# Optimization experiments

Hardware: AMD Instinct MI355X
Metric: run time of the kernel (lower is better)

The kernel has to match this reference:

```python
import jax, jax.numpy as jnp
import numpy as np


def setup_inputs() -> dict:
    key = jax.random.key(0)
    k1, k2, k3, k4 = jax.random.split(key, 4)
    B, S, D_in, D_state, D_out = 8, 2048, 1024, 1024, 1024
    x = jax.random.normal(k1, (B, S, D_in), dtype=jnp.float32)
    # A ~ rand * 0.1 (as in torch init)
    A = jax.random.uniform(k2, (D_state,), dtype=jnp.float32) * 0.1
    # B.weight ~ U(-0.01, 0.01)
    B_w = jax.random.uniform(k3, (D_state, D_in), dtype=jnp.float32, minval=-0.01, maxval=0.01)
    # linear_out: default torch Linear init (kaiming-uniform-ish); just use small uniform
    bound = 1.0 / np.sqrt(D_state)
    kw, kb = jax.random.split(k4)
    Wo = jax.random.uniform(kw, (D_out, D_state), dtype=jnp.float32, minval=-bound, maxval=bound)
    bo = jax.random.uniform(kb, (D_out,), dtype=jnp.float32, minval=-bound, maxval=bound)
    return {"x": x, "A": A, "B_w": B_w, "Wo": Wo, "bo": bo}


def reference(x, A, B_w, Wo, bo):
    # x: (B, S, D_in)
    Bsz = x.shape[0]
    D_state = A.shape[0]
    exp_decay = jnp.exp(-jnp.minimum(A, 10.0))  # (D_state,)
    # Precompute input projection in one batched matmul: (B, S, D_state)
    Bx = jnp.einsum("bsi,ni->bsn", x, B_w)

    def step(state, bx_t):
        # state: (B, D_state); bx_t: (B, D_state)
        state = jnp.tanh(exp_decay * state + bx_t)
        return state, state

    init = jnp.zeros((Bsz, D_state), dtype=x.dtype)
    # scan over time axis: move S to leading axis
    _, h = jax.lax.scan(step, init, jnp.swapaxes(Bx, 0, 1))  # h: (S, B, D_state)
    h = jnp.swapaxes(h, 0, 1)  # (B, S, D_state)
    out = jnp.einsum("bsn,on->bso", h, Wo) + bo
    return out
```

## Files before the change

### kernel.cpp

```cpp
#include <hip/hip_runtime.h>
#include <stdint.h>


typedef __attribute__((ext_vector_type(8))) short bf16x8;
typedef __attribute__((ext_vector_type(4))) float f32x4;
typedef __attribute__((ext_vector_type(8))) unsigned short u16x8;

#define C2F 2.88539008177792681472f
#define LOG2E 1.44269504088896340736f

static __device__ __forceinline__ unsigned short f2b(float f) {
  unsigned u = __builtin_bit_cast(unsigned, f);
  unsigned r = 0x7FFFu + ((u >> 16) & 1u);
  return (unsigned short)((u + r) >> 16);
}

static __device__ __forceinline__ void gload_lds16(const void* g, void* l) {
  __builtin_amdgcn_global_load_lds(
      (const __attribute__((address_space(1))) void*)(uintptr_t)g,
      (__attribute__((address_space(3))) void*)(unsigned)(uintptr_t)l,
      16, 0, 0);
}

__global__ __launch_bounds__(256) void cvt_f32_bf16(const float* __restrict__ in,
                                                    unsigned short* __restrict__ out,
                                                    float scale, int n8) {
  int i = blockIdx.x * 256 + threadIdx.x;
  if (i >= n8) return;
  const float4* p = (const float4*)in;
  float4 v0 = p[2 * (size_t)i];
  float4 v1 = p[2 * (size_t)i + 1];
  u16x8 o;
  o[0] = f2b(v0.x * scale); o[1] = f2b(v0.y * scale);
  o[2] = f2b(v0.z * scale); o[3] = f2b(v0.w * scale);
  o[4] = f2b(v1.x * scale); o[5] = f2b(v1.y * scale);
  o[6] = f2b(v1.z * scale); o[7] = f2b(v1.w * scale);
  *(u16x8*)(out + 8 * (size_t)i) = o;
}

__global__ __launch_bounds__(256) void dkc_kernel(const float* __restrict__ Av,
                                                  float* __restrict__ dkc, int n) {
  int i = blockIdx.x * 256 + threadIdx.x;
  if (i >= n) return;
  float a = fminf(Av[i], 10.0f);
  dkc[i] = C2F * __builtin_amdgcn_exp2f(-a * LOG2E);
}

__global__ __launch_bounds__(256) void bias2_kernel(const float* __restrict__ Wo,
                                                    const float* __restrict__ bo,
                                                    float* __restrict__ bias2) {
  const int o = blockIdx.x * 4 + (threadIdx.x >> 6);
  const int lane = threadIdx.x & 63;
  const float4* row = (const float4*)(Wo + (size_t)o * 1024);
  float s = 0.0f;
#pragma unroll
  for (int k = 0; k < 4; ++k) {
    float4 v = row[lane + k * 64];
    s += v.x + v.y + v.z + v.w;
  }
#pragma unroll
  for (int off = 32; off; off >>= 1) s += __shfl_down(s, off);
  if (lane == 0) bias2[o] = s + bo[o];
}

template <int MODE>
__global__ __launch_bounds__(512, 1) void gemm256(const unsigned short* __restrict__ A,
                                                  const unsigned short* __restrict__ B,
                                                  float* __restrict__ C,
                                                  const float* __restrict__ bv,
                                                  int M, int N, int K) {
  constexpr int BK = 32;
  __shared__ char lds[4][2][16384];
  const int tid = threadIdx.x;
  const int wave = tid >> 6, lane = tid & 63;
  const int wr = wave >> 2, wc = wave & 3;

  const int nbn = N >> 8;
  const int per = gridDim.x >> 3;
  const int tilei = (blockIdx.x & 7) * per + (blockIdx.x >> 3);
  const int m0 = (tilei / nbn) << 8;
  const int n0 = (tilei % nbn) << 8;

  int soff[2];
#pragma unroll
  for (int i = 0; i < 2; ++i) {
    int o = i * 8192 + wave * 1024 + lane * 16;
    int rp = o >> 7;
    int p = ((o >> 4) & 7) ^ (rp & 7);
    int row = rp * 2 + (p >> 2);
    int chunk = p & 3;
    soff[i] = row * K + chunk * 8;
  }
  const unsigned short* Abase = A + (size_t)m0 * K;
  const unsigned short* Bbase = B + (size_t)n0 * K;

#define STAGE(T_)                                                                \
  {                                                                              \
    const int _buf = (T_) & 3;                                                   \
    const int _k0 = (T_) * BK;                                                   \
    _Pragma("unroll") for (int i = 0; i < 2; ++i) {                              \
      gload_lds16(Abase + _k0 + soff[i], &lds[_buf][0][i * 8192 + wave * 1024]); \
      gload_lds16(Bbase + _k0 + soff[i], &lds[_buf][1][i * 8192 + wave * 1024]); \
    }                                                                            \
  }

  const int l15 = lane & 15, ck = lane >> 4;
  const int ra = wr * 128 + l15;
  const int rb = wc * 64 + l15;
  const int baseA = (ra >> 1) * 128 + ((((ra & 1) << 2) + ck) ^ ((ra >> 1) & 7)) * 16;
  const int baseB = (rb >> 1) * 128 + ((((rb & 1) << 2) + ck) ^ ((rb >> 1) & 7)) * 16;

  f32x4 acc[8][4] = {};

  STAGE(0); STAGE(1); STAGE(2);

  const int T = K / BK;

#define ITER(T_, WAITN, DOSTAGE)                                                  \
  {                                                                               \
    if (DOSTAGE) STAGE((T_) + 3);                                                 \
    asm volatile("s_waitcnt vmcnt(" #WAITN ")" ::: "memory");                     \
    __builtin_amdgcn_s_barrier();                                                 \
    const char* pa = &lds[(T_) & 3][0][baseA];                                    \
    const char* pb = &lds[(T_) & 3][1][baseB];                                    \
    bf16x8 bfr[4], af[4];                                                         \
    _Pragma("unroll") for (int nf = 0; nf < 4; ++nf)                              \
        bfr[nf] = *(const bf16x8*)(pb + nf * 1024);                               \
    _Pragma("unroll") for (int mf = 0; mf < 4; ++mf)                              \
        af[mf] = *(const bf16x8*)(pa + mf * 1024);                                \
    __builtin_amdgcn_s_setprio(1);                                                \
    _Pragma("unroll") for (int mf = 0; mf < 4; ++mf)                              \
      _Pragma("unroll") for (int nf = 0; nf < 4; ++nf)                            \
        acc[mf][nf] = __builtin_amdgcn_mfma_f32_16x16x32_bf16(af[mf], bfr[nf],    \
                                                              acc[mf][nf], 0, 0, 0); \
    __builtin_amdgcn_s_setprio(0);                                                \
    _Pragma("unroll") for (int mf = 0; mf < 4; ++mf)                              \
        af[mf] = *(const bf16x8*)(pa + (mf + 4) * 1024);                          \
    __builtin_amdgcn_s_setprio(1);                                                \
    _Pragma("unroll") for (int mf = 0; mf < 4; ++mf)                              \
      _Pragma("unroll") for (int nf = 0; nf < 4; ++nf)                            \
        acc[mf + 4][nf] = __builtin_amdgcn_mfma_f32_16x16x32_bf16(                \
            af[mf], bfr[nf], acc[mf + 4][nf], 0, 0, 0);                           \
    __builtin_amdgcn_s_setprio(0);                                                \
    __builtin_amdgcn_s_barrier();                                                 \
  }

  for (int t = 0; t < T - 3; ++t) ITER(t, 12, 1);
  ITER(T - 3, 8, 0);
  ITER(T - 2, 4, 0);
  ITER(T - 1, 0, 0);
#undef ITER
#undef STAGE

  const int cr = (lane >> 4) * 4;
  const int cc = lane & 15;
#pragma unroll
  for (int nf = 0; nf < 4; ++nf) {
    const int gc = n0 + wc * 64 + nf * 16 + cc;
    const float b = bv[gc];
#pragma unroll
    for (int mf = 0; mf < 8; ++mf) {
      const size_t base = (size_t)(m0 + wr * 128 + mf * 16 + cr) * N + gc;
#pragma unroll
      for (int r = 0; r < 4; ++r) {
        float v = MODE == 0 ? fmaf(acc[mf][nf][r], C2F, b) : (acc[mf][nf][r] + b);
        C[base + (size_t)r * N] = v;
      }
    }
  }
}

__global__ __launch_bounds__(256) void scan_kernel(const float* __restrict__ Bx,
                                                   const float* __restrict__ Av,
                                                   unsigned short* __restrict__ h) {
  constexpr int S = 2048, D = 1024, CHUNK = 256, W = 384;
  const int bid = blockIdx.x;
  const int half = bid & 1;
  const int chunk = (bid >> 1) & 7;
  const int b = bid >> 4;
  const int p = half * 256 + threadIdx.x;
  const unsigned n0 = 2u * p;

  const float2 av = *(const float2*)(Av + n0);
  const float m2dk0 = -2.0f * C2F * __builtin_amdgcn_exp2f(-fminf(av.x, 10.0f) * LOG2E);
  const float m2dk1 = -2.0f * C2F * __builtin_amdgcn_exp2f(-fminf(av.y, 10.0f) * LOG2E);

  const unsigned base = (unsigned)b * (S * D) + n0;
  const int t_store0 = chunk * CHUNK;
  const int t_start = (chunk * CHUNK - W) < 0 ? 0 : (chunk * CHUNK - W);
  const int t_end = t_store0 + CHUNK;

  float2 A[8], Bf[8];
#pragma unroll
  for (int j = 0; j < 8; ++j) A[j] = *(const float2*)(Bx + base + (unsigned)(t_start + j) * D);
#pragma unroll
  for (int j = 0; j < 8; ++j) Bf[j] = *(const float2*)(Bx + base + (unsigned)(t_start + 8 + j) * D);

  float r0 = 0.5f, r1 = 0.5f;

#define STEP2(CV)                                         \
  {                                                       \
    float w0 = fmaf(m2dk0, r0, (CV).x);                   \
    float w1 = fmaf(m2dk1, r1, (CV).y);                   \
    float e0 = __builtin_amdgcn_exp2f(w0);                \
    float e1 = __builtin_amdgcn_exp2f(w1);                \
    r0 = __builtin_amdgcn_rcpf(e0 + 1.0f);                \
    r1 = __builtin_amdgcn_rcpf(e1 + 1.0f);                \
  }

#define STORE2(T_)                                                        \
  {                                                                       \
    unsigned pk;                                                          \
    asm("v_cvt_pk_bf16_f32 %0, %1, %2" : "=v"(pk) : "v"(r0), "v"(r1));    \
    *(unsigned*)(h + base + (unsigned)(T_) * D) = pk;                     \
  }

  for (int t0 = t_start; t0 < t_store0; t0 += 16) {
#pragma unroll
    for (int j = 0; j < 8; ++j) STEP2(A[j]);
#pragma unroll
    for (int j = 0; j < 8; ++j) A[j] = *(const float2*)(Bx + base + (unsigned)(t0 + 16 + j) * D);
#pragma unroll
    for (int j = 0; j < 8; ++j) STEP2(Bf[j]);
#pragma unroll
    for (int j = 0; j < 8; ++j) Bf[j] = *(const float2*)(Bx + base + (unsigned)(t0 + 24 + j) * D);
  }
  for (int t0 = t_store0; t0 < t_end; t0 += 16) {
#pragma unroll
    for (int j = 0; j < 8; ++j) { STEP2(A[j]); STORE2(t0 + j); }
    if (t0 + 16 < t_end) {
#pragma unroll
      for (int j = 0; j < 8; ++j) A[j] = *(const float2*)(Bx + base + (unsigned)(t0 + 16 + j) * D);
    }
#pragma unroll
    for (int j = 0; j < 8; ++j) { STEP2(Bf[j]); STORE2(t0 + 8 + j); }
    if (t0 + 24 < t_end) {
#pragma unroll
      for (int j = 0; j < 8; ++j) Bf[j] = *(const float2*)(Bx + base + (unsigned)(t0 + 24 + j) * D);
    }
  }
#undef STEP2
#undef STORE2
}

extern "C" void kernel_launch(void* const* d_in, const int* in_sizes, int n_in,
                              void* d_out, int out_size, void* d_ws, size_t ws_size,
                              hipStream_t stream) {
  const float* x  = (const float*)d_in[0];
  const float* Av = (const float*)d_in[1];
  const float* Bw = (const float*)d_in[2];
  const float* Wo = (const float*)d_in[3];
  const float* bo = (const float*)d_in[4];
  float* out = (float*)d_out;

  const int Bsz = 8, S = 2048, Din = 1024, Dst = 1024, Dout = 1024;
  const int M = Bsz * S;

  char* ws = (char*)d_ws;
  unsigned short* x_bf  = (unsigned short*)ws;
  unsigned short* r_bf  = (unsigned short*)(ws + (size_t)M * Din * 2);
  unsigned short* Bw_bf = (unsigned short*)(ws + (size_t)M * Din * 4);
  unsigned short* Wo_bf = (unsigned short*)(ws + (size_t)M * Din * 4 + (size_t)Dst * Din * 2);
  float* dkc   = (float*)(ws + (size_t)M * Din * 4 + (size_t)Dst * Din * 4);
  float* bias2 = dkc + Dst;

  float* Bx = out;

  { int n8 = M * Din / 8;
    cvt_f32_bf16<<<(n8 + 255) / 256, 256, 0, stream>>>(x, x_bf, 1.0f, n8); }
  { int n8 = Dst * Din / 8;
    cvt_f32_bf16<<<(n8 + 255) / 256, 256, 0, stream>>>(Bw, Bw_bf, 1.0f, n8); }
  { int n8 = Dout * Dst / 8;
    cvt_f32_bf16<<<(n8 + 255) / 256, 256, 0, stream>>>(Wo, Wo_bf, -2.0f, n8); }
  dkc_kernel<<<4, 256, 0, stream>>>(Av, dkc, Dst);
  bias2_kernel<<<Dout / 4, 256, 0, stream>>>(Wo, bo, bias2);

  gemm256<0><<<dim3((M / 256) * (Dst / 256)), 512, 0, stream>>>(x_bf, Bw_bf, Bx, dkc, M, Dst, Din);
  scan_kernel<<<dim3(128), 256, 0, stream>>>(Bx, Av, r_bf);
  gemm256<1><<<dim3((M / 256) * (Dout / 256)), 512, 0, stream>>>(r_bf, Wo_bf, out, bias2, M, Dout, Dst);
}
```

Baseline: 148.5 us.

## Switch GEMM to double-buffered BK=64 pipeline with two blocks per CU

Replaces the 4-stage BK=32 LDS ring with a 2-stage BK=64 double buffer, keeping the same 128KB of LDS, and doubles the K work per barrier pair. It interleaves LDS fragment loads with MFMA groups and raises launch bounds to allow two blocks per CU. The aim is fewer barriers and better latency hiding. The cost is a shallower prefetch depth, and the second resident block may not fit given the LDS size and register pressure from holding more fragments.

```diff
diff --git a/kernel.cpp b/kernel.cpp
--- a/kernel.cpp
+++ b/kernel.cpp
@@ -64,13 +64,12 @@
 }
 
 template <int MODE>
-__global__ __launch_bounds__(512, 1) void gemm256(const unsigned short* __restrict__ A,
+__global__ __launch_bounds__(512, 2) void gemm256(const unsigned short* __restrict__ A,
                                                   const unsigned short* __restrict__ B,
                                                   float* __restrict__ C,
                                                   const float* __restrict__ bv,
                                                   int M, int N, int K) {
-  constexpr int BK = 32;
-  __shared__ char lds[4][2][16384];
+  __shared__ char lds[2][2][2][16384];
   const int tid = threadIdx.x;
   const int wave = tid >> 6, lane = tid & 63;
   const int wr = wave >> 2, wc = wave & 3;
@@ -94,14 +93,17 @@
   const unsigned short* Abase = A + (size_t)m0 * K;
   const unsigned short* Bbase = B + (size_t)n0 * K;
 
-#define STAGE(T_)                                                                \
-  {                                                                              \
-    const int _buf = (T_) & 3;                                                   \
-    const int _k0 = (T_) * BK;                                                   \
-    _Pragma("unroll") for (int i = 0; i < 2; ++i) {                              \
-      gload_lds16(Abase + _k0 + soff[i], &lds[_buf][0][i * 8192 + wave * 1024]); \
-      gload_lds16(Bbase + _k0 + soff[i], &lds[_buf][1][i * 8192 + wave * 1024]); \
-    }                                                                            \
+#define STAGE(T_)                                                                 \
+  {                                                                               \
+    const int _buf = (T_) & 1;                                                    \
+    const int _k0 = (T_) * 64;                                                    \
+    _Pragma("unroll") for (int ks = 0; ks < 2; ++ks)                              \
+      _Pragma("unroll") for (int i = 0; i < 2; ++i) {                             \
+        gload_lds16(Abase + _k0 + ks * 32 + soff[i],                              \
+                    &lds[_buf][0][ks][i * 8192 + wave * 1024]);                   \
+        gload_lds16(Bbase + _k0 + ks * 32 + soff[i],                              \
+                    &lds[_buf][1][ks][i * 8192 + wave * 1024]);                   \
+      }                                                                           \
   }
 
   const int l15 = lane & 15, ck = lane >> 4;
@@ -112,45 +114,66 @@
 
   f32x4 acc[8][4] = {};
 
-  STAGE(0); STAGE(1); STAGE(2);
-
-  const int T = K / BK;
-
-#define ITER(T_, WAITN, DOSTAGE)                                                  \
+#define MFMA_(a_, b_, c_) __builtin_amdgcn_mfma_f32_16x16x32_bf16(a_, b_, c_, 0, 0, 0)
+
+#define COMPUTE(BUF_)                                                             \
   {                                                                               \
-    if (DOSTAGE) STAGE((T_) + 3);                                                 \
-    asm volatile("s_waitcnt vmcnt(" #WAITN ")" ::: "memory");                     \
-    __builtin_amdgcn_s_barrier();                                                 \
-    const char* pa = &lds[(T_) & 3][0][baseA];                                    \
-    const char* pb = &lds[(T_) & 3][1][baseB];                                    \
-    bf16x8 bfr[4], af[4];                                                         \
+    const char* paA0 = &lds[BUF_][0][0][baseA];                                   \
+    const char* paA1 = &lds[BUF_][0][1][baseA];                                   \
+    const char* pbB0 = &lds[BUF_][1][0][baseB];                                   \
+    const char* pbB1 = &lds[BUF_][1][1][baseB];                                   \
+    bf16x8 b0[4], b1[4], alo[4], ahi[4], clo[4], chi[4];                          \
     _Pragma("unroll") for (int nf = 0; nf < 4; ++nf)                              \
-        bfr[nf] = *(const bf16x8*)(pb + nf * 1024);                               \
-    _Pragma("unroll") for (int mf = 0; mf < 4; ++mf)                              \
-        af[mf] = *(const bf16x8*)(pa + mf * 1024);                                \
+        b0[nf] = *(const bf16x8*)(pbB0 + nf * 1024);                              \
+    _Pragma("unroll") for (int mf = 0; mf < 4; ++mf)                              \
+        alo[mf] = *(const bf16x8*)(paA0 + mf * 1024);                             \
+    _Pragma("unroll") for (int mf = 0; mf < 4; ++mf)                              \
+        ahi[mf] = *(const bf16x8*)(paA0 + (mf + 4) * 1024);                       \
     __builtin_amdgcn_s_setprio(1);                                                \
     _Pragma("unroll") for (int mf = 0; mf < 4; ++mf)                              \
       _Pragma("unroll") for (int nf = 0; nf < 4; ++nf)                            \
-        acc[mf][nf] = __builtin_amdgcn_mfma_f32_16x16x32_bf16(af[mf], bfr[nf],    \
-                                                              acc[mf][nf], 0, 0, 0); \
+        acc[mf][nf] = MFMA_(alo[mf], b0[nf], acc[mf][nf]);                        \
     __builtin_amdgcn_s_setprio(0);                                                \
-    _Pragma("unroll") for (int mf = 0; mf < 4; ++mf)                              \
-        af[mf] = *(const bf16x8*)(pa + (mf + 4) * 1024);                          \
+    _Pragma("unroll") for (int nf = 0; nf < 4; ++nf)                              \
+        b1[nf] = *(const bf16x8*)(pbB1 + nf * 1024);                              \
+    _Pragma("unroll") for (int mf = 0; mf < 4; ++mf)                              \
+        clo[mf] = *(const bf16x8*)(paA1 + mf * 1024);                             \
     __builtin_amdgcn_s_setprio(1);                                                \
     _Pragma("unroll") for (int mf = 0; mf < 4; ++mf)                              \
       _Pragma("unroll") for (int nf = 0; nf < 4; ++nf)                            \
-        acc[mf + 4][nf] = __builtin_amdgcn_mfma_f32_16x16x32_bf16(                \
-            af[mf], bfr[nf], acc[mf + 4][nf], 0, 0, 0);                           \
+        acc[mf + 4][nf] = MFMA_(ahi[mf], b0[nf], acc[mf + 4][nf]);                \
     __builtin_amdgcn_s_setprio(0);                                                \
-    __builtin_amdgcn_s_barrier();                                                 \
-  }
-
-  for (int t = 0; t < T - 3; ++t) ITER(t, 12, 1);
-  ITER(T - 3, 8, 0);
-  ITER(T - 2, 4, 0);
-  ITER(T - 1, 0, 0);
-#undef ITER
+    _Pragma("unroll") for (int mf = 0; mf < 4; ++mf)                              \
+        chi[mf] = *(const bf16x8*)(paA1 + (mf + 4) * 1024);                       \
+    __builtin_amdgcn_s_setprio(1);                                                \
+    _Pragma("unroll") for (int mf = 0; mf < 4; ++mf)                              \
+      _Pragma("unroll") for (int nf = 0; nf < 4; ++nf)                            \
+        acc[mf][nf] = MFMA_(clo[mf], b1[nf], acc[mf][nf]);                        \
+    _Pragma("unroll") for (int mf = 0; mf < 4; ++mf)                              \
+      _Pragma("unroll") for (int nf = 0; nf < 4; ++nf)                            \
+        acc[mf + 4][nf] = MFMA_(chi[mf], b1[nf], acc[mf + 4][nf]);                \
+    __builtin_amdgcn_s_setprio(0);                                                \
+  }
+
+#define WAIT8 asm volatile("s_waitcnt vmcnt(8)" ::: "memory")
+#define WAIT0 asm volatile("s_waitcnt vmcnt(0)" ::: "memory")
+#define BAR __builtin_amdgcn_s_barrier()
+
+  const int T = K / 64;
+
+  STAGE(0);
+  for (int t = 0; t < T - 2; t += 2) {
+    STAGE(t + 1); WAIT8; BAR; COMPUTE(0); BAR;
+    STAGE(t + 2); WAIT8; BAR; COMPUTE(1); BAR;
+  }
+  STAGE(T - 1); WAIT8; BAR; COMPUTE(0); BAR;
+  WAIT0;        BAR; COMPUTE(1); BAR;
+
+#undef COMPUTE
 #undef STAGE
+#undef WAIT8
+#undef WAIT0
+#undef BAR
 
   const int cr = (lane >> 4) * 4;
   const int cc = lane & 15;
```

Result: slower. 153.6 us (+3.5%).

## Restructure GEMM main loop to double-buffered BK=64 with interleaved quadrant MFMAs

Applied to the files above, without the earlier changes.

Replaces the 4-stage BK=32 LDS ring with a 2-stage BK=64 double buffer. Each iteration is split into four quadrant MFMA phases, with global-to-LDS loads for the next tile issued between the phases. Launch bounds move to 2 blocks per CU to allow more occupancy, and LDS per block stays at 128KB. The goal is to overlap loads with compute more finely and cut barrier and waitcnt overhead per K step. The cost is more barriers per iteration and a full vmcnt(0) drain at the end of every step.

```diff
diff --git a/kernel.cpp b/kernel.cpp
--- a/kernel.cpp
+++ b/kernel.cpp
@@ -64,13 +64,12 @@
 }
 
 template <int MODE>
-__global__ __launch_bounds__(512, 1) void gemm256(const unsigned short* __restrict__ A,
+__global__ __launch_bounds__(512, 2) void gemm256(const unsigned short* __restrict__ A,
                                                   const unsigned short* __restrict__ B,
                                                   float* __restrict__ C,
                                                   const float* __restrict__ bv,
                                                   int M, int N, int K) {
-  constexpr int BK = 32;
-  __shared__ char lds[4][2][16384];
+  __shared__ char lds[2][2][2][16384];
   const int tid = threadIdx.x;
   const int wave = tid >> 6, lane = tid & 63;
   const int wr = wave >> 2, wc = wave & 3;
@@ -94,14 +93,14 @@
   const unsigned short* Abase = A + (size_t)m0 * K;
   const unsigned short* Bbase = B + (size_t)n0 * K;
 
-#define STAGE(T_)                                                                \
-  {                                                                              \
-    const int _buf = (T_) & 3;                                                   \
-    const int _k0 = (T_) * BK;                                                   \
-    _Pragma("unroll") for (int i = 0; i < 2; ++i) {                              \
-      gload_lds16(Abase + _k0 + soff[i], &lds[_buf][0][i * 8192 + wave * 1024]); \
-      gload_lds16(Bbase + _k0 + soff[i], &lds[_buf][1][i * 8192 + wave * 1024]); \
-    }                                                                            \
+#define STAGE_OP(T_, OP, SRC)                                                     \
+  {                                                                               \
+    const int _b = (T_) & 1;                                                      \
+    const int _k0 = (T_) * 64;                                                    \
+    _Pragma("unroll") for (int ks = 0; ks < 2; ++ks)                              \
+      _Pragma("unroll") for (int i = 0; i < 2; ++i)                               \
+        gload_lds16(SRC + _k0 + ks * 32 + soff[i],                                \
+                    &lds[_b][OP][ks][i * 8192 + wave * 1024]);                    \
   }
 
   const int l15 = lane & 15, ck = lane >> 4;
@@ -111,46 +110,72 @@
   const int baseB = (rb >> 1) * 128 + ((((rb & 1) << 2) + ck) ^ ((rb >> 1) & 7)) * 16;
 
   f32x4 acc[8][4] = {};
-
-  STAGE(0); STAGE(1); STAGE(2);
-
-  const int T = K / BK;
-
-#define ITER(T_, WAITN, DOSTAGE)                                                  \
-  {                                                                               \
-    if (DOSTAGE) STAGE((T_) + 3);                                                 \
-    asm volatile("s_waitcnt vmcnt(" #WAITN ")" ::: "memory");                     \
-    __builtin_amdgcn_s_barrier();                                                 \
-    const char* pa = &lds[(T_) & 3][0][baseA];                                    \
-    const char* pb = &lds[(T_) & 3][1][baseB];                                    \
-    bf16x8 bfr[4], af[4];                                                         \
-    _Pragma("unroll") for (int nf = 0; nf < 4; ++nf)                              \
-        bfr[nf] = *(const bf16x8*)(pb + nf * 1024);                               \
-    _Pragma("unroll") for (int mf = 0; mf < 4; ++mf)                              \
-        af[mf] = *(const bf16x8*)(pa + mf * 1024);                                \
-    __builtin_amdgcn_s_setprio(1);                                                \
-    _Pragma("unroll") for (int mf = 0; mf < 4; ++mf)                              \
-      _Pragma("unroll") for (int nf = 0; nf < 4; ++nf)                            \
-        acc[mf][nf] = __builtin_amdgcn_mfma_f32_16x16x32_bf16(af[mf], bfr[nf],    \
-                                                              acc[mf][nf], 0, 0, 0); \
-    __builtin_amdgcn_s_setprio(0);                                                \
-    _Pragma("unroll") for (int mf = 0; mf < 4; ++mf)                              \
-        af[mf] = *(const bf16x8*)(pa + (mf + 4) * 1024);                          \
-    __builtin_amdgcn_s_setprio(1);                                                \
-    _Pragma("unroll") for (int mf = 0; mf < 4; ++mf)                              \
-      _Pragma("unroll") for (int nf = 0; nf < 4; ++nf)                            \
-        acc[mf + 4][nf] = __builtin_amdgcn_mfma_f32_16x16x32_bf16(                \
-            af[mf], bfr[nf], acc[mf + 4][nf], 0, 0, 0);                           \
-    __builtin_amdgcn_s_setprio(0);                                                \
-    __builtin_amdgcn_s_barrier();                                                 \
-  }
-
-  for (int t = 0; t < T - 3; ++t) ITER(t, 12, 1);
-  ITER(T - 3, 8, 0);
-  ITER(T - 2, 4, 0);
-  ITER(T - 1, 0, 0);
-#undef ITER
-#undef STAGE
+  bf16x8 rA[8], rB0[4], rB1[4];
+
+#define RD_A(BUF, MH)                                                             \
+  _Pragma("unroll") for (int mf = 0; mf < 4; ++mf)                                \
+    _Pragma("unroll") for (int ks = 0; ks < 2; ++ks)                              \
+      rA[mf * 2 + ks] = *(const bf16x8*)(&lds[BUF][0][ks][baseA + ((MH)*4 + mf) * 1024]);
+
+#define RD_B(DST, BUF, NH)                                                        \
+  _Pragma("unroll") for (int i = 0; i < 2; ++i)                                   \
+    _Pragma("unroll") for (int ks = 0; ks < 2; ++ks)                              \
+      DST[i * 2 + ks] = *(const bf16x8*)(&lds[BUF][1][ks][baseB + ((NH)*2 + i) * 1024]);
+
+#define MFMA_(a_, b_, c_) __builtin_amdgcn_mfma_f32_16x16x32_bf16(a_, b_, c_, 0, 0, 0)
+
+#define MM(MH, NH, BREG)                                                          \
+  __builtin_amdgcn_s_setprio(1);                                                  \
+  _Pragma("unroll") for (int mf = 0; mf < 4; ++mf)                                \
+    _Pragma("unroll") for (int i = 0; i < 2; ++i)                                 \
+      _Pragma("unroll") for (int ks = 0; ks < 2; ++ks)                            \
+        acc[(MH)*4 + mf][(NH)*2 + i] =                                            \
+            MFMA_(rA[mf * 2 + ks], BREG[i * 2 + ks], acc[(MH)*4 + mf][(NH)*2 + i]); \
+  __builtin_amdgcn_s_setprio(0);
+
+#define BAR __builtin_amdgcn_s_barrier()
+#define LGKM0                                                                     \
+  do {                                                                            \
+    asm volatile("s_waitcnt lgkmcnt(0)" ::: "memory");                            \
+    __builtin_amdgcn_sched_barrier(0);                                            \
+  } while (0)
+#define VM0 asm volatile("s_waitcnt vmcnt(0)" ::: "memory")
+
+  const int T = K / 64;
+
+  STAGE_OP(0, 0, Abase);
+  STAGE_OP(0, 1, Bbase);
+  VM0; BAR;
+
+  for (int t = 0; t < T; ++t) {
+    const int cur = t & 1;
+    const bool st = (t + 1) < T;
+    RD_B(rB0, cur, 0);
+    RD_A(cur, 0);
+    if (st) STAGE_OP(t + 1, 0, Abase);
+    BAR; LGKM0;
+    MM(0, 0, rB0);
+    BAR;
+    RD_B(rB1, cur, 1);
+    if (st) STAGE_OP(t + 1, 1, Bbase);
+    BAR; LGKM0;
+    MM(0, 1, rB1);
+    BAR;
+    RD_A(cur, 1);
+    BAR; LGKM0;
+    MM(1, 1, rB1);
+    BAR;
+    MM(1, 0, rB0);
+    VM0; BAR;
+  }
+
+#undef STAGE_OP
+#undef RD_A
+#undef RD_B
+#undef MM
+#undef BAR
+#undef LGKM0
+#undef VM0
 
   const int cr = (lane >> 4) * 4;
   const int cc = lane & 15;
```

New measurement: 146.6 us. Within noise of the previous version (-1.3%).

## Restructure GEMM pipeline with paired phases, swapped MFMA operands, vectorized stores

Applied to the files above, without the earlier changes.

Reworks the GEMM main loop so that each phase loads all A and B fragments from LDS, waits for them, then issues all 32 MFMAs. The next stage's global-to-LDS loads are issued into the just-consumed slot after the barrier rather than before compute. MFMA operands are swapped so each lane holds four consecutive output columns, which allows float4 stores of C and a float4 bias load instead of scalar strided stores. Launch bounds now request two blocks per CU, which may constrain registers despite the larger fragment footprint.

```diff
diff --git a/kernel.cpp b/kernel.cpp
--- a/kernel.cpp
+++ b/kernel.cpp
@@ -64,12 +64,11 @@
 }
 
 template <int MODE>
-__global__ __launch_bounds__(512, 1) void gemm256(const unsigned short* __restrict__ A,
+__global__ __launch_bounds__(512, 2) void gemm256(const unsigned short* __restrict__ A,
                                                   const unsigned short* __restrict__ B,
                                                   float* __restrict__ C,
                                                   const float* __restrict__ bv,
                                                   int M, int N, int K) {
-  constexpr int BK = 32;
   __shared__ char lds[4][2][16384];
   const int tid = threadIdx.x;
   const int wave = tid >> 6, lane = tid & 63;
@@ -94,14 +93,12 @@
   const unsigned short* Abase = A + (size_t)m0 * K;
   const unsigned short* Bbase = B + (size_t)n0 * K;
 
-#define STAGE(T_)                                                                \
-  {                                                                              \
-    const int _buf = (T_) & 3;                                                   \
-    const int _k0 = (T_) * BK;                                                   \
-    _Pragma("unroll") for (int i = 0; i < 2; ++i) {                              \
-      gload_lds16(Abase + _k0 + soff[i], &lds[_buf][0][i * 8192 + wave * 1024]); \
-      gload_lds16(Bbase + _k0 + soff[i], &lds[_buf][1][i * 8192 + wave * 1024]); \
-    }                                                                            \
+#define STAGEP(SLOT, K0S)                                                         \
+  {                                                                               \
+    _Pragma("unroll") for (int i = 0; i < 2; ++i) {                               \
+      gload_lds16(Abase + (K0S) + soff[i], &lds[SLOT][0][i * 8192 + wave * 1024]); \
+      gload_lds16(Bbase + (K0S) + soff[i], &lds[SLOT][1][i * 8192 + wave * 1024]); \
+    }                                                                             \
   }
 
   const int l15 = lane & 15, ck = lane >> 4;
@@ -110,62 +107,66 @@
   const int baseA = (ra >> 1) * 128 + ((((ra & 1) << 2) + ck) ^ ((ra >> 1) & 7)) * 16;
   const int baseB = (rb >> 1) * 128 + ((((rb & 1) << 2) + ck) ^ ((rb >> 1) & 7)) * 16;
 
-  f32x4 acc[8][4] = {};
-
-  STAGE(0); STAGE(1); STAGE(2);
-
-  const int T = K / BK;
-
-#define ITER(T_, WAITN, DOSTAGE)                                                  \
+  f32x4 accT[4][8] = {};
+  bf16x8 rA[8], rB[4];
+
+#define MFMA_(a_, b_, c_) __builtin_amdgcn_mfma_f32_16x16x32_bf16(a_, b_, c_, 0, 0, 0)
+
+#define PHASE(SLOT, WAITN, DOSTAGE, K0S)                                          \
   {                                                                               \
-    if (DOSTAGE) STAGE((T_) + 3);                                                 \
-    asm volatile("s_waitcnt vmcnt(" #WAITN ")" ::: "memory");                     \
+    asm volatile("s_waitcnt vmcnt(" WAITN ")" ::: "memory");                      \
     __builtin_amdgcn_s_barrier();                                                 \
-    const char* pa = &lds[(T_) & 3][0][baseA];                                    \
-    const char* pb = &lds[(T_) & 3][1][baseB];                                    \
-    bf16x8 bfr[4], af[4];                                                         \
-    _Pragma("unroll") for (int nf = 0; nf < 4; ++nf)                              \
-        bfr[nf] = *(const bf16x8*)(pb + nf * 1024);                               \
-    _Pragma("unroll") for (int mf = 0; mf < 4; ++mf)                              \
-        af[mf] = *(const bf16x8*)(pa + mf * 1024);                                \
+    _Pragma("unroll") for (int f = 0; f < 4; ++f)                                 \
+        rB[f] = *(const bf16x8*)(&lds[SLOT][1][baseB + f * 1024]);                \
+    _Pragma("unroll") for (int f = 0; f < 8; ++f)                                 \
+        rA[f] = *(const bf16x8*)(&lds[SLOT][0][baseA + f * 1024]);                \
+    asm volatile("s_waitcnt lgkmcnt(0)" ::: "memory");                            \
+    __builtin_amdgcn_sched_barrier(0);                                            \
     __builtin_amdgcn_s_setprio(1);                                                \
-    _Pragma("unroll") for (int mf = 0; mf < 4; ++mf)                              \
+    _Pragma("unroll") for (int mf = 0; mf < 8; ++mf)                              \
       _Pragma("unroll") for (int nf = 0; nf < 4; ++nf)                            \
-        acc[mf][nf] = __builtin_amdgcn_mfma_f32_16x16x32_bf16(af[mf], bfr[nf],    \
-                                                              acc[mf][nf], 0, 0, 0); \
-    __builtin_amdgcn_s_setprio(0);                                                \
-    _Pragma("unroll") for (int mf = 0; mf < 4; ++mf)                              \
-        af[mf] = *(const bf16x8*)(pa + (mf + 4) * 1024);                          \
-    __builtin_amdgcn_s_setprio(1);                                                \
-    _Pragma("unroll") for (int mf = 0; mf < 4; ++mf)                              \
-      _Pragma("unroll") for (int nf = 0; nf < 4; ++nf)                            \
-        acc[mf + 4][nf] = __builtin_amdgcn_mfma_f32_16x16x32_bf16(                \
-            af[mf], bfr[nf], acc[mf + 4][nf], 0, 0, 0);                           \
+        accT[nf][mf] = MFMA_(rB[nf], rA[mf], accT[nf][mf]);                       \
     __builtin_amdgcn_s_setprio(0);                                                \
     __builtin_amdgcn_s_barrier();                                                 \
-  }
-
-  for (int t = 0; t < T - 3; ++t) ITER(t, 12, 1);
-  ITER(T - 3, 8, 0);
-  ITER(T - 2, 4, 0);
-  ITER(T - 1, 0, 0);
-#undef ITER
-#undef STAGE
-
-  const int cr = (lane >> 4) * 4;
-  const int cc = lane & 15;
+    if (DOSTAGE) STAGEP(SLOT, K0S);                                               \
+  }
+
+  const int T = K / 64;
+
+  STAGEP(0, 0); STAGEP(1, 32); STAGEP(2, 64); STAGEP(3, 96);
+
+  for (int t = 0; t < T - 2; ++t) {
+    const int sa = (t & 1) * 2;
+    PHASE(sa,     "12", true, t * 64 + 128);
+    PHASE(sa + 1, "12", true, t * 64 + 160);
+  }
+  {
+    const int sa = ((T - 2) & 1) * 2;
+    PHASE(sa,     "12", false, 0);
+    PHASE(sa + 1, "8",  false, 0);
+  }
+  {
+    const int sa = ((T - 1) & 1) * 2;
+    PHASE(sa,     "4",  false, 0);
+    PHASE(sa + 1, "0",  false, 0);
+  }
+
+#undef PHASE
+#undef STAGEP
+#undef MFMA_
+
+  const int cm = lane & 15;
+  const int cn = (lane >> 4) * 4;
 #pragma unroll
   for (int nf = 0; nf < 4; ++nf) {
-    const int gc = n0 + wc * 64 + nf * 16 + cc;
-    const float b = bv[gc];
+    const int gn = n0 + wc * 64 + nf * 16 + cn;
+    const f32x4 bb = *(const f32x4*)(bv + gn);
 #pragma unroll
     for (int mf = 0; mf < 8; ++mf) {
-      const size_t base = (size_t)(m0 + wr * 128 + mf * 16 + cr) * N + gc;
-#pragma unroll
-      for (int r = 0; r < 4; ++r) {
-        float v = MODE == 0 ? fmaf(acc[mf][nf][r], C2F, b) : (acc[mf][nf][r] + b);
-        C[base + (size_t)r * N] = v;
-      }
+      const int gm = m0 + wr * 128 + mf * 16 + cm;
+      f32x4 v = accT[nf][mf];
+      if (MODE == 0) v = v * C2F + bb; else v = v + bb;
+      *(f32x4*)(C + (size_t)gm * N + gn) = v;
     }
   }
 }
```

Measured after the change: 147.5 us. Within noise of the previous version (-0.7%).
